# Kernel optimization log

Measured on AMD Instinct MI355X. Metric: run time of the kernel, lower is better.

The kernel has to match this reference:

```python
import jax, jax.numpy as jnp
import numpy as np

B, S, D_MODEL = 2, 2048, 512
KEY_DIM, VALUE_DIM, OUTPUT_DIM, NUM_HEADS = 256, 256, 512, 8


def setup_inputs() -> dict:
    key = jax.random.key(0)
    ks = jax.random.split(key, 12)
    s = 0.02
    return {
        "V": jax.random.normal(ks[0], (B, S, D_MODEL), jnp.float32),
        "Q": jax.random.normal(ks[1], (B, S, D_MODEL), jnp.float32),
        "K": jax.random.normal(ks[2], (B, S, D_MODEL), jnp.float32),
        "mask": jax.random.normal(ks[3], (B, 1, S, S), jnp.float32),
        "Wq": jax.random.normal(ks[4], (D_MODEL, KEY_DIM), jnp.float32) * s,
        "bq": jnp.zeros((KEY_DIM,), jnp.float32),
        "Wk": jax.random.normal(ks[5], (D_MODEL, KEY_DIM), jnp.float32) * s,
        "bk": jnp.zeros((KEY_DIM,), jnp.float32),
        "Wv": jax.random.normal(ks[6], (D_MODEL, VALUE_DIM), jnp.float32) * s,
        "bv": jnp.zeros((VALUE_DIM,), jnp.float32),
        "Wo": jax.random.normal(ks[7], (VALUE_DIM, OUTPUT_DIM), jnp.float32) * s,
        "bo": jnp.zeros((OUTPUT_DIM,), jnp.float32),
    }


def _split_heads(x, num_heads):
    # [B, S, H*d] -> [B, H, S, d]
    b, s, hd = x.shape
    return x.reshape(b, s, num_heads, hd // num_heads).transpose(0, 2, 1, 3)


def reference(V, Q, K, mask, Wq, bq, Wk, bk, Wv, bv, Wo, bo):
    denom = jnp.sqrt(jnp.float32(KEY_DIM))  # NOTE: full key_dim, as in source
    q = _split_heads(Q @ Wq + bq, NUM_HEADS)  # [B,H,S,dk]
    k = _split_heads(K @ Wk + bk, NUM_HEADS)
    scores = jnp.einsum("bhqd,bhkd->bhqk", q, k) / denom
    scores = scores + mask  # soft (additive) mask
    weights = jax.nn.softmax(scores, axis=-1)
    v = _split_heads(V @ Wv + bv, NUM_HEADS)  # [B,H,S,dv]
    ctx = jnp.einsum("bhqk,bhkd->bhqd", weights, v)  # [B,H,S,dv]
    b, h, s, d = ctx.shape
    ctx = ctx.transpose(0, 2, 1, 3).reshape(b, s, h * d)  # merge heads
    return ctx @ Wo + bo
```

## Files before the change

kernel.cpp:

```cpp
#include <hip/hip_runtime.h>

typedef __attribute__((ext_vector_type(8))) short bf16x8;
typedef __attribute__((ext_vector_type(4))) float f32x4;

#define B_  2
#define S_  2048
#define DM  512
#define KD  256
#define HD  32
#define NH  8

__device__ __forceinline__ float bf2f(ushort u) {
    return __uint_as_float(((uint)u) << 16);
}
__device__ __forceinline__ ushort f2bf(float f) {
    uint x = __float_as_uint(f);
    return (ushort)((x + 0x7fffu + ((x >> 16) & 1u)) >> 16);
}
#define MFMA __builtin_amdgcn_mfma_f32_16x16x32_bf16

__device__ __forceinline__ int detect_isbf(const ushort* __restrict__ q)
{
    int lane = threadIdx.x & 63;
    int e = (q[lane] >> 7) & 0xFF;
    unsigned long long m = __ballot(e >= 100 && e <= 133);
    return __popcll(m) >= 58;
}

__global__ __launch_bounds__(256) void transpose_w(
    const void* __restrict__ Wq, const void* __restrict__ Wk, const void* __restrict__ Wv,
    const void* __restrict__ Wo,
    const void* __restrict__ bq, const void* __restrict__ bk,
    const void* __restrict__ bv, const void* __restrict__ bo,
    const ushort* __restrict__ qsrc,
    ushort* __restrict__ Wt, ushort* __restrict__ Wot, float* __restrict__ biasf)
{
    int isbf = detect_isbf(qsrc);
    int bid = blockIdx.x;
    if (bid >= 512) {
        for (int i = threadIdx.x; i < 1280; i += 256) {
            const void* bp; int off;
            if (i < 256)      { bp = bq; off = i; }
            else if (i < 512) { bp = bk; off = i - 256; }
            else if (i < 768) { bp = bv; off = i - 512; }
            else              { bp = bo; off = i - 768; }
            biasf[i] = isbf ? bf2f(((const ushort*)bp)[off]) : ((const float*)bp)[off];
        }
        return;
    }
    const void* W; int R, C; ushort* T;
    int m = bid >> 7, tix = bid & 127;
    if (m < 3) { W = (m == 0) ? Wq : (m == 1) ? Wk : Wv; R = 512; C = 256; T = Wt + m * 131072; }
    else       { W = Wo; R = 256; C = 512; T = Wot; }
    int tilesPerRow = C >> 5;
    int r0 = (tix / tilesPerRow) * 32, c0 = (tix % tilesPerRow) * 32;
    __shared__ float lds[32][33];
    int t = threadIdx.x;
    int rr = t >> 3, cc = (t & 7) * 4;
    if (isbf) {
        const ushort* Ws = (const ushort*)W;
        #pragma unroll
        for (int j = 0; j < 4; ++j) lds[rr][cc + j] = bf2f(Ws[(size_t)(r0 + rr) * C + c0 + cc + j]);
    } else {
        float4 v = *(const float4*)((const float*)W + (size_t)(r0 + rr) * C + c0 + cc);
        lds[rr][cc + 0] = v.x; lds[rr][cc + 1] = v.y; lds[rr][cc + 2] = v.z; lds[rr][cc + 3] = v.w;
    }
    __syncthreads();
    ushort4 o;
    o.x = f2bf(lds[cc + 0][rr]); o.y = f2bf(lds[cc + 1][rr]);
    o.z = f2bf(lds[cc + 2][rr]); o.w = f2bf(lds[cc + 3][rr]);
    int n = c0 + rr, k = r0 + cc;
    *(ushort4*)(T + ((((size_t)(n >> 4) * (R >> 3) + (k >> 3)) * 16 + (n & 15)) << 3) + (k & 7)) = o;
}

__global__ __launch_bounds__(256) void qkv_gemm(
    const void* __restrict__ Q, const void* __restrict__ K, const void* __restrict__ V,
    const ushort* __restrict__ Wt, const float* __restrict__ biasf,
    ushort* __restrict__ qh, ushort* __restrict__ kh, ushort* __restrict__ vT)
{
    int isbf = detect_isbf((const ushort*)Q);
    int y = blockIdx.y;
    const void* X = (y == 0) ? Q : (y == 1) ? K : V;
    int wave = threadIdx.x >> 6, lane = threadIdx.x & 63;
    int l16 = lane & 15, quad = lane >> 4;
    int m0 = blockIdx.x * 32;
    int n0 = wave * 64;
    const ushort* W = Wt + (size_t)y * (256 * 512);

    auto loadA = [&](int ks, bf16x8* a) {
        #pragma unroll
        for (int i = 0; i < 2; ++i) {
            if (isbf) {
                a[i] = *(const bf16x8*)((const ushort*)X + (size_t)(m0 + 16 * i + l16) * 512 + ks + quad * 8);
            } else {
                const float* p = (const float*)X + (size_t)(m0 + 16 * i + l16) * 512 + ks + quad * 8;
                float4 f0 = *(const float4*)p, f1 = *(const float4*)(p + 4);
                bf16x8 v8;
                v8[0] = (short)f2bf(f0.x); v8[1] = (short)f2bf(f0.y);
                v8[2] = (short)f2bf(f0.z); v8[3] = (short)f2bf(f0.w);
                v8[4] = (short)f2bf(f1.x); v8[5] = (short)f2bf(f1.y);
                v8[6] = (short)f2bf(f1.z); v8[7] = (short)f2bf(f1.w);
                a[i] = v8;
            }
        }
    };
    auto loadB = [&](int ks, bf16x8* b) {
        #pragma unroll
        for (int j = 0; j < 4; ++j)
            b[j] = *(const bf16x8*)(W + (((size_t)((n0 >> 4) + j) * 64 + (ks >> 3) + quad) * 16 + l16) * 8);
    };

    f32x4 acc[2][4] = {};
    bf16x8 aC[2], bC[4], aN[2], bN[4];
    loadA(0, aC); loadB(0, bC);
    for (int ks = 0; ks < 512; ks += 32) {
        if (ks + 32 < 512) { loadA(ks + 32, aN); loadB(ks + 32, bN); }
        #pragma unroll
        for (int i = 0; i < 2; ++i)
            #pragma unroll
            for (int j = 0; j < 4; ++j)
                acc[i][j] = MFMA(aC[i], bC[j], acc[i][j], 0, 0, 0);
        aC[0] = aN[0]; aC[1] = aN[1];
        #pragma unroll
        for (int j = 0; j < 4; ++j) bC[j] = bN[j];
    }
    if (y < 2) {
        ushort* out = (y == 0) ? qh : kh;
        #pragma unroll
        for (int i = 0; i < 2; ++i) {
            #pragma unroll
            for (int j = 0; j < 4; ++j) {
                int n = n0 + 16 * j + l16;
                float bs = biasf[y * 256 + n];
                int h = n >> 5, d = n & 31;
                #pragma unroll
                for (int r = 0; r < 4; ++r) {
                    int rg = m0 + 16 * i + quad * 4 + r;
                    int bb = rg >> 11, ss = rg & 2047;
                    out[((((size_t)bb * NH + h) * S_ + ss) << 5) + d] = f2bf(acc[i][j][r] + bs);
                }
            }
        }
    } else {
        #pragma unroll
        for (int i = 0; i < 2; ++i) {
            int rg0 = m0 + 16 * i + quad * 4;
            int bb = rg0 >> 11, s0 = rg0 & 2047;
            #pragma unroll
            for (int j = 0; j < 4; ++j) {
                int n = n0 + 16 * j + l16;
                float bs = biasf[2 * 256 + n];
                int h = n >> 5, d = n & 31;
                ushort4 o;
                o.x = f2bf(acc[i][j][0] + bs); o.y = f2bf(acc[i][j][1] + bs);
                o.z = f2bf(acc[i][j][2] + bs); o.w = f2bf(acc[i][j][3] + bs);
                *(ushort4*)(vT + (((size_t)(bb * NH + h) * HD + d) * S_) + s0) = o;
            }
        }
    }
}

__global__ __launch_bounds__(256) void attn(
    const ushort* __restrict__ qh, const ushort* __restrict__ kh,
    const ushort* __restrict__ vT, const void* __restrict__ maskp,
    float* __restrict__ pO, float* __restrict__ pl)
{
    __shared__ __align__(16) ushort ldsP[4][2][16][72];
    int isbf;
    {
        int lane = threadIdx.x & 63;
        ushort u = ((const ushort*)maskp)[lane];
        int e = (u >> 7) & 0xFF;
        unsigned long long m = __ballot(e >= 100 && e <= 133);
        isbf = __popcll(m) >= 58;
    }
    int wave = threadIdx.x >> 6, lane = threadIdx.x & 63;
    int l16 = lane & 15, quad = lane >> 4;
    int wid = blockIdx.x * 4 + wave;
    int chunk = wid & 1, qt32 = (wid >> 1) & 63, bh = wid >> 7;
    int b = bh >> 3;
    int q0 = qt32 * 32;
    const ushort* qb = qh + (size_t)bh * S_ * HD;
    const ushort* kb = kh + (size_t)bh * S_ * HD;
    const ushort* vb = vT + (size_t)bh * HD * S_;
    const ushort* mbb = (const ushort*)maskp + (size_t)b * S_ * S_;
    const float*  mbf = (const float*)maskp  + (size_t)b * S_ * S_;
    size_t mbase = (size_t)(q0 + quad * 4) * S_ + l16;

    bf16x8 aq0 = *(const bf16x8*)(qb + (size_t)(q0 + l16) * HD + quad * 8);
    bf16x8 aq1 = *(const bf16x8*)(qb + (size_t)(q0 + 16 + l16) * HD + quad * 8);
    f32x4 O00 = {0,0,0,0}, O01 = {0,0,0,0}, O10 = {0,0,0,0}, O11 = {0,0,0,0};
    const f32x4 zero = {0, 0, 0, 0};
    float lsum0[4] = {0,0,0,0}, lsum1[4] = {0,0,0,0};
    float M0[16], M1[16];
    bf16x8 Vf[4];

    auto loadK = [&](int k0, bf16x8* Kf) {
        #pragma unroll
        for (int c = 0; c < 4; ++c)
            Kf[c] = *(const bf16x8*)(kb + (size_t)(k0 + c * 16 + l16) * HD + quad * 8);
    };
    auto loadM = [&](int k0) {
        if (isbf) {
            #pragma unroll
            for (int r = 0; r < 4; ++r) {
                const ushort* p = mbb + mbase + (size_t)r * S_ + k0;
                #pragma unroll
                for (int c = 0; c < 4; ++c) M0[c * 4 + r] = bf2f(p[c * 16]);
                p += (size_t)16 * S_;
                #pragma unroll
                for (int c = 0; c < 4; ++c) M1[c * 4 + r] = bf2f(p[c * 16]);
            }
        } else {
            #pragma unroll
            for (int r = 0; r < 4; ++r) {
                const float* p = mbf + mbase + (size_t)r * S_ + k0;
                #pragma unroll
                for (int c = 0; c < 4; ++c) M0[c * 4 + r] = p[c * 16];
                p += (size_t)16 * S_;
                #pragma unroll
                for (int c = 0; c < 4; ++c) M1[c * 4 + r] = p[c * 16];
            }
        }
    };
    auto loadV = [&](int k0) {
        Vf[0] = *(const bf16x8*)(vb + (size_t)l16 * S_ + k0 + quad * 8);
        Vf[1] = *(const bf16x8*)(vb + (size_t)l16 * S_ + k0 + 32 + quad * 8);
        Vf[2] = *(const bf16x8*)(vb + (size_t)(16 + l16) * S_ + k0 + quad * 8);
        Vf[3] = *(const bf16x8*)(vb + (size_t)(16 + l16) * S_ + k0 + 32 + quad * 8);
    };

    auto substep = [&](bf16x8* Kcur, int nextk0, bf16x8* Knext) {
        if (nextk0 >= 0) loadK(nextk0, Knext);
        f32x4 Sc0[4], Sc1[4];
        #pragma unroll
        for (int c = 0; c < 4; ++c) Sc0[c] = MFMA(aq0, Kcur[c], zero, 0, 0, 0);
        #pragma unroll
        for (int c = 0; c < 4; ++c) Sc1[c] = MFMA(aq1, Kcur[c], zero, 0, 0, 0);
        #pragma unroll
        for (int c = 0; c < 4; ++c) {
            #pragma unroll
            for (int r = 0; r < 4; ++r) {
                float s = fminf(fmaf(Sc0[c][r], 0.0625f, M0[c * 4 + r]), 30.0f);
                float p = __expf(s);
                lsum0[r] += p;
                ldsP[wave][0][quad * 4 + r][c * 16 + l16] = f2bf(p);
                float s1 = fminf(fmaf(Sc1[c][r], 0.0625f, M1[c * 4 + r]), 30.0f);
                float p1 = __expf(s1);
                lsum1[r] += p1;
                ldsP[wave][1][quad * 4 + r][c * 16 + l16] = f2bf(p1);
            }
        }
        if (nextk0 >= 0) loadM(nextk0);
        asm volatile("s_waitcnt lgkmcnt(0)" ::: "memory");
        bf16x8 aP00 = *(const bf16x8*)&ldsP[wave][0][l16][quad * 8];
        bf16x8 aP01 = *(const bf16x8*)&ldsP[wave][0][l16][32 + quad * 8];
        bf16x8 aP10 = *(const bf16x8*)&ldsP[wave][1][l16][quad * 8];
        bf16x8 aP11 = *(const bf16x8*)&ldsP[wave][1][l16][32 + quad * 8];
        O00 = MFMA(aP00, Vf[0], O00, 0, 0, 0);
        O00 = MFMA(aP01, Vf[1], O00, 0, 0, 0);
        O01 = MFMA(aP00, Vf[2], O01, 0, 0, 0);
        O01 = MFMA(aP01, Vf[3], O01, 0, 0, 0);
        O10 = MFMA(aP10, Vf[0], O10, 0, 0, 0);
        O10 = MFMA(aP11, Vf[1], O10, 0, 0, 0);
        O11 = MFMA(aP10, Vf[2], O11, 0, 0, 0);
        O11 = MFMA(aP11, Vf[3], O11, 0, 0, 0);
        if (nextk0 >= 0) loadV(nextk0);
    };

    int kbase = chunk * 1024;
    bf16x8 Ka[4], Kb2[4];
    loadK(kbase, Ka); loadM(kbase); loadV(kbase);
    for (int t = 0; t < 16; t += 2) {
        substep(Ka, kbase + (t + 1) * 64, Kb2);
        substep(Kb2, (t + 2 < 16) ? kbase + (t + 2) * 64 : -1, Ka);
    }

    #pragma unroll
    for (int tile = 0; tile < 2; ++tile) {
        int wid16 = ((bh * 128) + (qt32 * 2 + tile)) * 2 + chunk;
        float* po = pO + (size_t)wid16 * 512;
        f32x4 Oa = tile ? O10 : O00, Ob = tile ? O11 : O01;
        float* ls = tile ? lsum1 : lsum0;
        #pragma unroll
        for (int r = 0; r < 4; ++r) {
            int row = quad * 4 + r;
            po[row * 32 + l16]      = Oa[r];
            po[row * 32 + 16 + l16] = Ob[r];
            float sthis = ls[r];
            #pragma unroll
            for (int off = 8; off; off >>= 1) sthis += __shfl_xor(sthis, off, 16);
            if (l16 == 0) pl[wid16 * 16 + row] = sthis;
        }
    }
}

__global__ __launch_bounds__(256) void out_proj(
    const float* __restrict__ pO, const float* __restrict__ pl,
    const ushort* __restrict__ Wot, const float* __restrict__ biasf,
    float* __restrict__ out)
{
    int wave = threadIdx.x >> 6, lane = threadIdx.x & 63;
    int l16 = lane & 15, quad = lane >> 4;
    int m0 = (blockIdx.x >> 1) * 32;
    int n0 = (blockIdx.x & 1) * 256 + wave * 64;
    f32x4 acc[2][4] = {};
    for (int ks = 0; ks < 256; ks += 32) {
        int h = ks >> 5;
        bf16x8 a[2], b[4];
        #pragma unroll
        for (int i = 0; i < 2; ++i) {
            int row = m0 + 16 * i + l16;
            int bb = row >> 11, s = row & 2047;
            int qt = s >> 4, r16 = s & 15;
            int wid0 = ((bb * NH + h) << 8) | (qt << 1);
            const float* p0 = pO + (size_t)wid0 * 512 + r16 * 32 + quad * 8;
            float4 x0 = *(const float4*)p0,         x1 = *(const float4*)(p0 + 4);
            float4 y0 = *(const float4*)(p0 + 512), y1 = *(const float4*)(p0 + 516);
            float il = 1.0f / (pl[wid0 * 16 + r16] + pl[(wid0 + 1) * 16 + r16]);
            bf16x8 v8;
            v8[0] = (short)f2bf((x0.x + y0.x) * il); v8[1] = (short)f2bf((x0.y + y0.y) * il);
            v8[2] = (short)f2bf((x0.z + y0.z) * il); v8[3] = (short)f2bf((x0.w + y0.w) * il);
            v8[4] = (short)f2bf((x1.x + y1.x) * il); v8[5] = (short)f2bf((x1.y + y1.y) * il);
            v8[6] = (short)f2bf((x1.z + y1.z) * il); v8[7] = (short)f2bf((x1.w + y1.w) * il);
            a[i] = v8;
        }
        #pragma unroll
        for (int j = 0; j < 4; ++j)
            b[j] = *(const bf16x8*)(Wot + (((size_t)((n0 >> 4) + j) * 32 + (ks >> 3) + quad) * 16 + l16) * 8);
        #pragma unroll
        for (int i = 0; i < 2; ++i)
            #pragma unroll
            for (int j = 0; j < 4; ++j)
                acc[i][j] = MFMA(a[i], b[j], acc[i][j], 0, 0, 0);
    }
    #pragma unroll
    for (int i = 0; i < 2; ++i) {
        #pragma unroll
        for (int j = 0; j < 4; ++j) {
            int n = n0 + 16 * j + l16;
            float bs = biasf[768 + n];
            #pragma unroll
            for (int r = 0; r < 4; ++r) {
                int rg = m0 + 16 * i + quad * 4 + r;
                out[(size_t)rg * DM + n] = acc[i][j][r] + bs;
            }
        }
    }
}

extern "C" void kernel_launch(void* const* d_in, const int* in_sizes, int n_in,
                              void* d_out, int out_size, void* d_ws, size_t ws_size,
                              hipStream_t stream)
{
    const void* V    = d_in[0];
    const void* Q    = d_in[1];
    const void* K    = d_in[2];
    const void* mask = d_in[3];
    const void* Wq = d_in[4];  const void* bq = d_in[5];
    const void* Wk = d_in[6];  const void* bk = d_in[7];
    const void* Wv = d_in[8];  const void* bv = d_in[9];
    const void* Wo = d_in[10]; const void* bo = d_in[11];
    float* out = (float*)d_out;

    char* ws = (char*)d_ws;
    float*  biasf = (float*)ws;
    ushort* Wt  = (ushort*)(ws + 8192);
    ushort* Wot = Wt  + 393216;
    ushort* qh  = Wot + 131072;
    ushort* kh  = qh  + 1048576;
    ushort* vT  = kh  + 1048576;
    float*  pO  = (float*)(vT + 1048576);
    float*  pl  = pO + 4096 * 512;

    transpose_w<<<513, 256, 0, stream>>>(Wq, Wk, Wv, Wo, bq, bk, bv, bo,
                                         (const ushort*)Q, Wt, Wot, biasf);
    qkv_gemm<<<dim3(128, 3), 256, 0, stream>>>(Q, K, V, Wt, biasf, qh, kh, vT);
    attn<<<512, 256, 0, stream>>>(qh, kh, vT, mask, pO, pl);
    out_proj<<<256, 256, 0, stream>>>(pO, pl, Wot, biasf, out);
}
```

Baseline: 189.5 us.

## Halve GEMM row tiles, use packed bf16 convert, drop softmax clamp

The QKV projection and output projection kernels now compute 16-row tiles instead of 32, which doubles their grid sizes so more blocks fill the GPU. Float-to-bf16 conversions in the GEMM loaders and in the attention probability path now use the hardware v_cvt_pk_bf16_f32 instruction in place of software rounding. The fminf clamp at 30 before exp in the attention softmax is removed. Smaller tiles give less weight reuse per block, and removing the clamp could overflow exp if scores plus mask grow large.

New measurement: 172.9 us. -8.8%, faster.

```diff
diff --git a/kernel.cpp b/kernel.cpp
--- a/kernel.cpp
+++ b/kernel.cpp
@@ -16,6 +16,11 @@
 __device__ __forceinline__ ushort f2bf(float f) {
     uint x = __float_as_uint(f);
     return (ushort)((x + 0x7fffu + ((x >> 16) & 1u)) >> 16);
+}
+__device__ __forceinline__ uint cvt_pk_bf16(float lo, float hi) {
+    uint r;
+    asm("v_cvt_pk_bf16_f32 %0, %1, %2" : "=v"(r) : "v"(lo), "v"(hi));
+    return r;
 }
 #define MFMA __builtin_amdgcn_mfma_f32_16x16x32_bf16
 
@@ -83,25 +88,22 @@
     const void* X = (y == 0) ? Q : (y == 1) ? K : V;
     int wave = threadIdx.x >> 6, lane = threadIdx.x & 63;
     int l16 = lane & 15, quad = lane >> 4;
-    int m0 = blockIdx.x * 32;
+    int m0 = blockIdx.x * 16;
     int n0 = wave * 64;
     const ushort* W = Wt + (size_t)y * (256 * 512);
 
     auto loadA = [&](int ks, bf16x8* a) {
-        #pragma unroll
-        for (int i = 0; i < 2; ++i) {
-            if (isbf) {
-                a[i] = *(const bf16x8*)((const ushort*)X + (size_t)(m0 + 16 * i + l16) * 512 + ks + quad * 8);
-            } else {
-                const float* p = (const float*)X + (size_t)(m0 + 16 * i + l16) * 512 + ks + quad * 8;
-                float4 f0 = *(const float4*)p, f1 = *(const float4*)(p + 4);
-                bf16x8 v8;
-                v8[0] = (short)f2bf(f0.x); v8[1] = (short)f2bf(f0.y);
-                v8[2] = (short)f2bf(f0.z); v8[3] = (short)f2bf(f0.w);
-                v8[4] = (short)f2bf(f1.x); v8[5] = (short)f2bf(f1.y);
-                v8[6] = (short)f2bf(f1.z); v8[7] = (short)f2bf(f1.w);
-                a[i] = v8;
-            }
+        if (isbf) {
+            *a = *(const bf16x8*)((const ushort*)X + (size_t)(m0 + l16) * 512 + ks + quad * 8);
+        } else {
+            const float* p = (const float*)X + (size_t)(m0 + l16) * 512 + ks + quad * 8;
+            float4 f0 = *(const float4*)p, f1 = *(const float4*)(p + 4);
+            union { uint u[4]; bf16x8 v; } cv;
+            cv.u[0] = cvt_pk_bf16(f0.x, f0.y);
+            cv.u[1] = cvt_pk_bf16(f0.z, f0.w);
+            cv.u[2] = cvt_pk_bf16(f1.x, f1.y);
+            cv.u[3] = cvt_pk_bf16(f1.z, f1.w);
+            *a = cv.v;
         }
     };
     auto loadB = [&](int ks, bf16x8* b) {
@@ -110,52 +112,44 @@
             b[j] = *(const bf16x8*)(W + (((size_t)((n0 >> 4) + j) * 64 + (ks >> 3) + quad) * 16 + l16) * 8);
     };
 
-    f32x4 acc[2][4] = {};
-    bf16x8 aC[2], bC[4], aN[2], bN[4];
-    loadA(0, aC); loadB(0, bC);
+    f32x4 acc[4] = {};
+    bf16x8 aC, bC[4], aN, bN[4];
+    loadA(0, &aC); loadB(0, bC);
     for (int ks = 0; ks < 512; ks += 32) {
-        if (ks + 32 < 512) { loadA(ks + 32, aN); loadB(ks + 32, bN); }
-        #pragma unroll
-        for (int i = 0; i < 2; ++i)
-            #pragma unroll
-            for (int j = 0; j < 4; ++j)
-                acc[i][j] = MFMA(aC[i], bC[j], acc[i][j], 0, 0, 0);
-        aC[0] = aN[0]; aC[1] = aN[1];
+        if (ks + 32 < 512) { loadA(ks + 32, &aN); loadB(ks + 32, bN); }
+        #pragma unroll
+        for (int j = 0; j < 4; ++j)
+            acc[j] = MFMA(aC, bC[j], acc[j], 0, 0, 0);
+        aC = aN;
         #pragma unroll
         for (int j = 0; j < 4; ++j) bC[j] = bN[j];
     }
     if (y < 2) {
         ushort* out = (y == 0) ? qh : kh;
         #pragma unroll
-        for (int i = 0; i < 2; ++i) {
-            #pragma unroll
-            for (int j = 0; j < 4; ++j) {
-                int n = n0 + 16 * j + l16;
-                float bs = biasf[y * 256 + n];
-                int h = n >> 5, d = n & 31;
-                #pragma unroll
-                for (int r = 0; r < 4; ++r) {
-                    int rg = m0 + 16 * i + quad * 4 + r;
-                    int bb = rg >> 11, ss = rg & 2047;
-                    out[((((size_t)bb * NH + h) * S_ + ss) << 5) + d] = f2bf(acc[i][j][r] + bs);
-                }
+        for (int j = 0; j < 4; ++j) {
+            int n = n0 + 16 * j + l16;
+            float bs = biasf[y * 256 + n];
+            int h = n >> 5, d = n & 31;
+            #pragma unroll
+            for (int r = 0; r < 4; ++r) {
+                int rg = m0 + quad * 4 + r;
+                int bb = rg >> 11, ss = rg & 2047;
+                out[((((size_t)bb * NH + h) * S_ + ss) << 5) + d] = f2bf(acc[j][r] + bs);
             }
         }
     } else {
-        #pragma unroll
-        for (int i = 0; i < 2; ++i) {
-            int rg0 = m0 + 16 * i + quad * 4;
-            int bb = rg0 >> 11, s0 = rg0 & 2047;
-            #pragma unroll
-            for (int j = 0; j < 4; ++j) {
-                int n = n0 + 16 * j + l16;
-                float bs = biasf[2 * 256 + n];
-                int h = n >> 5, d = n & 31;
-                ushort4 o;
-                o.x = f2bf(acc[i][j][0] + bs); o.y = f2bf(acc[i][j][1] + bs);
-                o.z = f2bf(acc[i][j][2] + bs); o.w = f2bf(acc[i][j][3] + bs);
-                *(ushort4*)(vT + (((size_t)(bb * NH + h) * HD + d) * S_) + s0) = o;
-            }
+        int rg0 = m0 + quad * 4;
+        int bb = rg0 >> 11, s0 = rg0 & 2047;
+        #pragma unroll
+        for (int j = 0; j < 4; ++j) {
+            int n = n0 + 16 * j + l16;
+            float bs = biasf[2 * 256 + n];
+            int h = n >> 5, d = n & 31;
+            ushort4 o;
+            o.x = f2bf(acc[j][0] + bs); o.y = f2bf(acc[j][1] + bs);
+            o.z = f2bf(acc[j][2] + bs); o.w = f2bf(acc[j][3] + bs);
+            *(ushort4*)(vT + (((size_t)(bb * NH + h) * HD + d) * S_) + s0) = o;
         }
     }
 }
@@ -239,16 +233,22 @@
         for (int c = 0; c < 4; ++c) Sc1[c] = MFMA(aq1, Kcur[c], zero, 0, 0, 0);
         #pragma unroll
         for (int c = 0; c < 4; ++c) {
+            float p0v[4], p1v[4];
             #pragma unroll
             for (int r = 0; r < 4; ++r) {
-                float s = fminf(fmaf(Sc0[c][r], 0.0625f, M0[c * 4 + r]), 30.0f);
-                float p = __expf(s);
-                lsum0[r] += p;
-                ldsP[wave][0][quad * 4 + r][c * 16 + l16] = f2bf(p);
-                float s1 = fminf(fmaf(Sc1[c][r], 0.0625f, M1[c * 4 + r]), 30.0f);
-                float p1 = __expf(s1);
-                lsum1[r] += p1;
-                ldsP[wave][1][quad * 4 + r][c * 16 + l16] = f2bf(p1);
+                float p = __expf(fmaf(Sc0[c][r], 0.0625f, M0[c * 4 + r]));
+                lsum0[r] += p; p0v[r] = p;
+                float q = __expf(fmaf(Sc1[c][r], 0.0625f, M1[c * 4 + r]));
+                lsum1[r] += q; p1v[r] = q;
+            }
+            #pragma unroll
+            for (int r = 0; r < 4; r += 2) {
+                uint w0 = cvt_pk_bf16(p0v[r], p0v[r + 1]);
+                ldsP[wave][0][quad * 4 + r][c * 16 + l16]     = (ushort)w0;
+                ldsP[wave][0][quad * 4 + r + 1][c * 16 + l16] = (ushort)(w0 >> 16);
+                uint w1 = cvt_pk_bf16(p1v[r], p1v[r + 1]);
+                ldsP[wave][1][quad * 4 + r][c * 16 + l16]     = (ushort)w1;
+                ldsP[wave][1][quad * 4 + r + 1][c * 16 + l16] = (ushort)(w1 >> 16);
             }
         }
         if (nextk0 >= 0) loadM(nextk0);
@@ -302,15 +302,14 @@
 {
     int wave = threadIdx.x >> 6, lane = threadIdx.x & 63;
     int l16 = lane & 15, quad = lane >> 4;
-    int m0 = (blockIdx.x >> 1) * 32;
+    int m0 = (blockIdx.x >> 1) * 16;
     int n0 = (blockIdx.x & 1) * 256 + wave * 64;
-    f32x4 acc[2][4] = {};
+    f32x4 acc[4] = {};
     for (int ks = 0; ks < 256; ks += 32) {
         int h = ks >> 5;
-        bf16x8 a[2], b[4];
-        #pragma unroll
-        for (int i = 0; i < 2; ++i) {
-            int row = m0 + 16 * i + l16;
+        bf16x8 a, b[4];
+        {
+            int row = m0 + l16;
             int bb = row >> 11, s = row & 2047;
             int qt = s >> 4, r16 = s & 15;
             int wid0 = ((bb * NH + h) << 8) | (qt << 1);
@@ -318,33 +317,28 @@
             float4 x0 = *(const float4*)p0,         x1 = *(const float4*)(p0 + 4);
             float4 y0 = *(const float4*)(p0 + 512), y1 = *(const float4*)(p0 + 516);
             float il = 1.0f / (pl[wid0 * 16 + r16] + pl[(wid0 + 1) * 16 + r16]);
-            bf16x8 v8;
-            v8[0] = (short)f2bf((x0.x + y0.x) * il); v8[1] = (short)f2bf((x0.y + y0.y) * il);
-            v8[2] = (short)f2bf((x0.z + y0.z) * il); v8[3] = (short)f2bf((x0.w + y0.w) * il);
-            v8[4] = (short)f2bf((x1.x + y1.x) * il); v8[5] = (short)f2bf((x1.y + y1.y) * il);
-            v8[6] = (short)f2bf((x1.z + y1.z) * il); v8[7] = (short)f2bf((x1.w + y1.w) * il);
-            a[i] = v8;
+            union { uint u[4]; bf16x8 v; } cv;
+            cv.u[0] = cvt_pk_bf16((x0.x + y0.x) * il, (x0.y + y0.y) * il);
+            cv.u[1] = cvt_pk_bf16((x0.z + y0.z) * il, (x0.w + y0.w) * il);
+            cv.u[2] = cvt_pk_bf16((x1.x + y1.x) * il, (x1.y + y1.y) * il);
+            cv.u[3] = cvt_pk_bf16((x1.z + y1.z) * il, (x1.w + y1.w) * il);
+            a = cv.v;
         }
         #pragma unroll
         for (int j = 0; j < 4; ++j)
             b[j] = *(const bf16x8*)(Wot + (((size_t)((n0 >> 4) + j) * 32 + (ks >> 3) + quad) * 16 + l16) * 8);
         #pragma unroll
-        for (int i = 0; i < 2; ++i)
-            #pragma unroll
-            for (int j = 0; j < 4; ++j)
-                acc[i][j] = MFMA(a[i], b[j], acc[i][j], 0, 0, 0);
+        for (int j = 0; j < 4; ++j)
+            acc[j] = MFMA(a, b[j], acc[j], 0, 0, 0);
     }
     #pragma unroll
-    for (int i = 0; i < 2; ++i) {
-        #pragma unroll
-        for (int j = 0; j < 4; ++j) {
-            int n = n0 + 16 * j + l16;
-            float bs = biasf[768 + n];
-            #pragma unroll
-            for (int r = 0; r < 4; ++r) {
-                int rg = m0 + 16 * i + quad * 4 + r;
-                out[(size_t)rg * DM + n] = acc[i][j][r] + bs;
-            }
+    for (int j = 0; j < 4; ++j) {
+        int n = n0 + 16 * j + l16;
+        float bs = biasf[768 + n];
+        #pragma unroll
+        for (int r = 0; r < 4; ++r) {
+            int rg = m0 + quad * 4 + r;
+            out[(size_t)rg * DM + n] = acc[j][r] + bs;
         }
     }
 }
@@ -375,7 +369,7 @@
 
     transpose_w<<<513, 256, 0, stream>>>(Wq, Wk, Wv, Wo, bq, bk, bv, bo,
                                          (const ushort*)Q, Wt, Wot, biasf);
-    qkv_gemm<<<dim3(128, 3), 256, 0, stream>>>(Q, K, V, Wt, biasf, qh, kh, vT);
+    qkv_gemm<<<dim3(256, 3), 256, 0, stream>>>(Q, K, V, Wt, biasf, qh, kh, vT);
     attn<<<512, 256, 0, stream>>>(qh, kh, vT, mask, pO, pl);
-    out_proj<<<256, 256, 0, stream>>>(pO, pl, Wot, biasf, out);
-}
+    out_proj<<<512, 256, 0, stream>>>(pO, pl, Wot, biasf, out);
+}
```
